# Kernel optimization log

Measured on AMD Instinct MI355X. Metric: run time of the kernel, lower is better.

The kernel has to match this reference:

```python
import jax, jax.numpy as jnp
import numpy as np

B, S, D = 2, 2048, 1024
H = 16
DH = D // H  # 64

def setup_inputs() -> dict:
    key = jax.random.key(0)
    k1, k2, k3, k4 = jax.random.split(key, 4)
    scale = 0.02
    x = jax.random.normal(k1, (B, S, D), dtype=jnp.float32)
    W_query = jax.random.normal(k2, (D, D), dtype=jnp.float32) * scale
    W_key = jax.random.normal(k3, (D, D), dtype=jnp.float32) * scale
    W_value = jax.random.normal(k4, (D, D), dtype=jnp.float32) * scale
    return {"x": x, "W_query": W_query, "W_key": W_key, "W_value": W_value}

def reference(x, W_query, W_key, W_value):
    b, n, d_in = x.shape
    # project and split heads: [b, h, n, dh]
    q = (x @ W_query).reshape(b, n, H, DH).transpose(0, 2, 1, 3)
    k = (x @ W_key).reshape(b, n, H, DH).transpose(0, 2, 1, 3)
    v = (x @ W_value).reshape(b, n, H, DH).transpose(0, 2, 1, 3)
    # raw scores, then causal mask (strict upper triangle -> -inf)
    scores = jnp.einsum('bhqd,bhkd->bhqk', q, k)
    causal = jnp.tril(jnp.ones((n, n), dtype=bool))  # True = keep
    scores = jnp.where(causal, scores, -jnp.inf)
    weights = jax.nn.softmax(scores / jnp.sqrt(jnp.float32(DH)), axis=-1)
    ctx = jnp.einsum('bhqk,bhkd->bhqd', weights, v)
    return ctx.transpose(0, 2, 1, 3).reshape(b, n, H * DH)
```

## Files before the change

kernel.cpp:

```cpp
#include <hip/hip_runtime.h>
#include <hip/hip_bf16.h>

#define S_LEN   2048
#define D_MODEL 1024
#define N_HEADS 16
#define D_HEAD  64
#define HEAD_ELEMS (2048ull * 64ull)
#define MAT_ELEMS  (4096ull * 1024ull)
#define W_ELEMS    (1024ull * 1024ull)

typedef __attribute__((ext_vector_type(8))) short short8_t;
typedef __attribute__((ext_vector_type(4))) short short4_t;
typedef __attribute__((ext_vector_type(4))) float f32x4;

__device__ __forceinline__ short f2bf(float f) {
    __hip_bfloat16 h = __float2bfloat16(f);
    union { __hip_bfloat16 h; short s; } cv;
    cv.h = h;
    return cv.s;
}

#define GLD_LDS16(gptr, lptr) \
    __builtin_amdgcn_global_load_lds( \
        (const __attribute__((address_space(1))) unsigned int*)(gptr), \
        (__attribute__((address_space(3))) unsigned int*)(lptr), 16, 0, 0)

__global__ __launch_bounds__(256) void convert_x_kernel(
    const float* __restrict__ x, short* __restrict__ xb)
{
    const int i = (blockIdx.x * 256 + threadIdx.x) * 8;
    const float4 v0 = *(const float4*)(x + i);
    const float4 v1 = *(const float4*)(x + i + 4);
    short8_t u;
    u[0] = f2bf(v0.x); u[1] = f2bf(v0.y); u[2] = f2bf(v0.z); u[3] = f2bf(v0.w);
    u[4] = f2bf(v1.x); u[5] = f2bf(v1.y); u[6] = f2bf(v1.z); u[7] = f2bf(v1.w);
    *(short8_t*)(xb + i) = u;
}

__global__ __launch_bounds__(256) void transpose_w_kernel(
    const float* __restrict__ Wq, const float* __restrict__ Wk,
    const float* __restrict__ Wv, short* __restrict__ wt)
{
    const int k0 = blockIdx.x * 64;
    const int n0 = blockIdx.y * 64;
    const int which = blockIdx.z;
    const float* W = (which == 0) ? Wq : (which == 1) ? Wk : Wv;
    short* out = wt + (size_t)which * W_ELEMS;

    __shared__ float Ts[64][68];
    const int t = threadIdx.x;
    {
        const int c4 = (t & 15) * 4;
#pragma unroll
        for (int i = 0; i < 4; ++i) {
            const int r = (t >> 4) + i * 16;
            const float4 v = *(const float4*)(W + (size_t)(k0 + r) * D_MODEL + n0 + c4);
            Ts[c4 + 0][r] = v.x; Ts[c4 + 1][r] = v.y;
            Ts[c4 + 2][r] = v.z; Ts[c4 + 3][r] = v.w;
        }
    }
    __syncthreads();
    const int nl = t >> 2;
#pragma unroll
    for (int s = 0; s < 2; ++s) {
        const int koff = (t & 3) * 8 + s * 32;
        short8_t u;
#pragma unroll
        for (int j = 0; j < 8; ++j) u[j] = f2bf(Ts[nl][koff + j]);
        *(short8_t*)(out + (size_t)(n0 + nl) * D_MODEL + k0 + koff) = u;
    }
}

__global__ __launch_bounds__(256, 3) void qkv_mfma_gemm_kernel(
    const short* __restrict__ xb,
    const short* __restrict__ wt,
    short* __restrict__ qkv)
{
    const int mBlock = blockIdx.x * 128;
    const int nBlock = blockIdx.y * 128;
    const int which  = blockIdx.z;
    const short* Bt = wt + (size_t)which * W_ELEMS;
    short* outBase  = qkv + (size_t)which * MAT_ELEMS;

    __shared__ short As[128 * 32];
    __shared__ short Bs[128 * 32];
    __shared__ __align__(16) short Es[4][64 * 72];

    const int t    = threadIdx.x;
    const int w    = t >> 6;
    const int lane = t & 63;
    const int n16  = lane & 15;
    const int quad = lane >> 4;
    const int mq   = (w & 1) * 64;
    const int nq   = (w >> 1) * 64;

    f32x4 acc[4][4];
#pragma unroll
    for (int i = 0; i < 4; ++i)
#pragma unroll
        for (int j = 0; j < 4; ++j) acc[i][j] = (f32x4){0.f, 0.f, 0.f, 0.f};

    const int off0 = w * 2048 + lane * 16;
    const int off1 = off0 + 1024;
    const int r0s = off0 >> 6, k0s = (off0 & 63) >> 1;
    const int r1s = off1 >> 6, k1s = (off1 & 63) >> 1;
    const short* gA0 = xb + (size_t)(mBlock + r0s) * D_MODEL + k0s;
    const short* gA1 = xb + (size_t)(mBlock + r1s) * D_MODEL + k1s;
    const short* gB0 = Bt + (size_t)(nBlock + r0s) * D_MODEL + k0s;
    const short* gB1 = Bt + (size_t)(nBlock + r1s) * D_MODEL + k1s;
    short* lA0 = As + w * 1024;
    short* lA1 = As + w * 1024 + 512;
    short* lB0 = Bs + w * 1024;
    short* lB1 = Bs + w * 1024 + 512;

    for (int k0 = 0; k0 < D_MODEL; k0 += 32) {
        __syncthreads();
        GLD_LDS16(gA0 + k0, lA0);
        GLD_LDS16(gA1 + k0, lA1);
        GLD_LDS16(gB0 + k0, lB0);
        GLD_LDS16(gB1 + k0, lB1);
        __syncthreads();

        short8_t af[4], bf[4];
#pragma unroll
        for (int mt = 0; mt < 4; ++mt)
            af[mt] = *(const short8_t*)&As[(mq + mt * 16 + n16) * 32 + quad * 8];
#pragma unroll
        for (int nt = 0; nt < 4; ++nt)
            bf[nt] = *(const short8_t*)&Bs[(nq + nt * 16 + n16) * 32 + quad * 8];
#pragma unroll
        for (int mt = 0; mt < 4; ++mt)
#pragma unroll
            for (int nt = 0; nt < 4; ++nt)
                acc[mt][nt] = __builtin_amdgcn_mfma_f32_16x16x32_bf16(
                    af[mt], bf[nt], acc[mt][nt], 0, 0, 0);
    }

    const float oscale = (which == 0) ? 0.125f * 1.44269504089f : 1.0f;
    if (which < 2) {
        short* E = &Es[w][0];
#pragma unroll
        for (int mt = 0; mt < 4; ++mt)
#pragma unroll
            for (int nt = 0; nt < 4; ++nt) {
                const int dhl = nt * 16 + n16;
#pragma unroll
                for (int reg = 0; reg < 4; ++reg) {
                    const int ml = mt * 16 + quad * 4 + reg;
                    E[ml * 72 + dhl] = f2bf(acc[mt][nt][reg] * oscale);
                }
            }
        const int h  = (nBlock + nq) >> 6;
        const int m0 = mBlock + mq;
        const int bb = m0 >> 11, ss0 = m0 & 2047;
        const int rsub = lane >> 3;
        const int ch   = lane & 7;
        short* orow = outBase + ((size_t)(bb * N_HEADS + h) * S_LEN + ss0) * D_HEAD
                      + ch * 8;
#pragma unroll
        for (int it = 0; it < 8; ++it) {
            const int row = it * 8 + rsub;
            const short8_t v = *(const short8_t*)&E[row * 72 + ch * 8];
            *(short8_t*)(orow + (size_t)row * D_HEAD) = v;
        }
    } else {
#pragma unroll
        for (int mt = 0; mt < 4; ++mt) {
            const int m0 = mBlock + mq + mt * 16 + quad * 4;
            const int bb = m0 >> 11, ss0 = m0 & 2047;
#pragma unroll
            for (int nt = 0; nt < 4; ++nt) {
                const int n = nBlock + nq + nt * 16 + n16;
                const int h = n >> 6, dh = n & 63;
                short4_t u;
                u[0] = f2bf(acc[mt][nt][0]); u[1] = f2bf(acc[mt][nt][1]);
                u[2] = f2bf(acc[mt][nt][2]); u[3] = f2bf(acc[mt][nt][3]);
                *(short4_t*)(outBase +
                    ((size_t)((bb * N_HEADS + h) * D_HEAD + dh)) * S_LEN + ss0) = u;
            }
        }
    }
}

__global__ __launch_bounds__(256, 4) void attn_mfma_kernel(
    const short* __restrict__ qkv,
    float* __restrict__ out)
{
    const int bh   = blockIdx.x;
    const int qb   = 31 - blockIdx.y;
    const int t    = threadIdx.x;
    const int w    = t >> 6;
    const int lane = t & 63;
    const int n    = lane & 15;
    const int quad = lane >> 4;

    const short* Q  = qkv + (size_t)bh * HEAD_ELEMS;
    const short* K  = qkv + MAT_ELEMS + (size_t)bh * HEAD_ELEMS;
    const short* Vt = qkv + 2 * MAT_ELEMS + (size_t)bh * HEAD_ELEMS;

    __shared__ __align__(16) short Ks[64 * 64];
    __shared__ __align__(16) short Vs[64 * 64];
    __shared__ __align__(16) short Ps[4][16][72];

    const int srow0 = w * 16 + (lane >> 3);
    const int srow1 = srow0 + 8;
    const int sd0 = ((lane & 7) ^ (srow0 & 7)) * 8;
    const int sd1 = ((lane & 7) ^ (srow1 & 7)) * 8;
    const short* gK0 = K + srow0 * 64 + sd0;
    const short* gK1 = K + srow1 * 64 + sd1;
    const short* gV0 = Vt + (size_t)srow0 * S_LEN + sd0;
    const short* gV1 = Vt + (size_t)srow1 * S_LEN + sd1;
    short* lK0 = Ks + (w * 16) * 64;
    short* lK1 = Ks + (w * 16 + 8) * 64;
    short* lV0 = Vs + (w * 16) * 64;
    short* lV1 = Vs + (w * 16 + 8) * 64;

    const int pcK = ((quad ^ (n & 7))) * 8;

    const int bb = bh >> 4;
    const int hh = bh & 15;

    const int r0   = qb * 64 + w * 16;
    const int qrow = r0 + n;

    const short8_t bq0 = *(const short8_t*)(Q + (size_t)qrow * D_HEAD + quad * 8);
    const short8_t bq1 = *(const short8_t*)(Q + (size_t)qrow * D_HEAD + quad * 8 + 32);

    float m = -__builtin_inff();
    float l = 0.f;
    f32x4 o[4];
#pragma unroll
    for (int f = 0; f < 4; ++f) o[f] = (f32x4){0.f, 0.f, 0.f, 0.f};

    for (int tile = 0; tile <= qb; ++tile) {
        const int j0 = tile * 64;
        __syncthreads();
        GLD_LDS16(gK0 + j0 * 64, lK0);
        GLD_LDS16(gK1 + j0 * 64, lK1);
        GLD_LDS16(gV0 + j0, lV0);
        GLD_LDS16(gV1 + j0, lV1);
        __syncthreads();

        f32x4 st[4];
        __builtin_amdgcn_s_setprio(1);
#pragma unroll
        for (int kg = 0; kg < 4; ++kg) {
            const int rbase = (kg * 16 + n) * 64;
            const short8_t a0 = *(const short8_t*)&Ks[rbase + pcK];
            const short8_t a1 = *(const short8_t*)&Ks[rbase + (pcK ^ 32)];
            f32x4 acc = (f32x4){0.f, 0.f, 0.f, 0.f};
            acc = __builtin_amdgcn_mfma_f32_16x16x32_bf16(a0, bq0, acc, 0, 0, 0);
            acc = __builtin_amdgcn_mfma_f32_16x16x32_bf16(a1, bq1, acc, 0, 0, 0);
            st[kg] = acc;
        }
        __builtin_amdgcn_s_setprio(0);

        float p[16];
        float mx = -__builtin_inff();
        if (tile == qb) {
#pragma unroll
            for (int kg = 0; kg < 4; ++kg)
#pragma unroll
                for (int r = 0; r < 4; ++r) {
                    const int key = j0 + kg * 16 + quad * 4 + r;
                    float s = st[kg][r];
                    s = (key <= qrow) ? s : -__builtin_inff();
                    p[kg * 4 + r] = s;
                    mx = fmaxf(mx, s);
                }
        } else {
#pragma unroll
            for (int i = 0; i < 16; ++i) {
                const float s = st[i >> 2][i & 3];
                p[i] = s;
                mx = fmaxf(mx, s);
            }
        }
        mx = fmaxf(mx, __shfl_xor(mx, 16));
        mx = fmaxf(mx, __shfl_xor(mx, 32));

        float ls = 0.f;
        if (__all(mx <= m + 8.0f)) {
#pragma unroll
            for (int i = 0; i < 16; ++i) {
                p[i] = __builtin_amdgcn_exp2f(p[i] - m);
                ls += p[i];
            }
            ls += __shfl_xor(ls, 16);
            ls += __shfl_xor(ls, 32);
            l += ls;
        } else {
            const float mnew  = fmaxf(m, mx);
            const float alpha = __builtin_amdgcn_exp2f(m - mnew);
#pragma unroll
            for (int i = 0; i < 16; ++i) {
                p[i] = __builtin_amdgcn_exp2f(p[i] - mnew);
                ls += p[i];
            }
            ls += __shfl_xor(ls, 16);
            ls += __shfl_xor(ls, 32);
            l = l * alpha + ls;
            m = mnew;
#pragma unroll
            for (int f = 0; f < 4; ++f) {
                o[f][0] *= alpha; o[f][1] *= alpha;
                o[f][2] *= alpha; o[f][3] *= alpha;
            }
        }

#pragma unroll
        for (int kg = 0; kg < 4; ++kg) {
            const unsigned int b0 = __builtin_bit_cast(unsigned int, p[kg * 4 + 0]);
            const unsigned int b1 = __builtin_bit_cast(unsigned int, p[kg * 4 + 1]);
            const unsigned int b2 = __builtin_bit_cast(unsigned int, p[kg * 4 + 2]);
            const unsigned int b3 = __builtin_bit_cast(unsigned int, p[kg * 4 + 3]);
            uint2 pk;
            pk.x = (b0 >> 16) | (b1 & 0xffff0000u);
            pk.y = (b2 >> 16) | (b3 & 0xffff0000u);
            *(uint2*)&Ps[w][n][kg * 16 + quad * 4] = pk;
        }
        const short8_t pb0 = *(const short8_t*)&Ps[w][n][quad * 8];
        const short8_t pb1 = *(const short8_t*)&Ps[w][n][quad * 8 + 32];

        __builtin_amdgcn_s_setprio(1);
#pragma unroll
        for (int f = 0; f < 4; ++f) {
            const int rbase = (f * 16 + n) * 64;
            const short8_t va0 = *(const short8_t*)&Vs[rbase + pcK];
            const short8_t va1 = *(const short8_t*)&Vs[rbase + (pcK ^ 32)];
            o[f] = __builtin_amdgcn_mfma_f32_16x16x32_bf16(va0, pb0, o[f], 0, 0, 0);
            o[f] = __builtin_amdgcn_mfma_f32_16x16x32_bf16(va1, pb1, o[f], 0, 0, 0);
        }
        __builtin_amdgcn_s_setprio(0);
    }

    __syncthreads();
    float* Os = (float*)((w < 2) ? (void*)Ks : (void*)Vs) + (w & 1) * 1024;
    const float inv_l = 1.0f / l;
#pragma unroll
    for (int f = 0; f < 4; ++f) {
        const int c  = f * 4 + quad;
        const int pc = c ^ n;
        f32x4 q4;
        q4[0] = o[f][0] * inv_l; q4[1] = o[f][1] * inv_l;
        q4[2] = o[f][2] * inv_l; q4[3] = o[f][3] * inv_l;
        *(f32x4*)&Os[n * 64 + pc * 4] = q4;
    }
#pragma unroll
    for (int rr = 0; rr < 4; ++rr) {
        const int row = rr * 4 + quad;
        const int pc  = n ^ row;
        const f32x4 val = *(const f32x4*)&Os[row * 64 + pc * 4];
        *(f32x4*)(out + ((size_t)(bb * S_LEN + r0 + row)) * D_MODEL
                      + hh * D_HEAD + n * 4) = val;
    }
}

extern "C" void kernel_launch(void* const* d_in, const int* in_sizes, int n_in,
                              void* d_out, int out_size, void* d_ws, size_t ws_size,
                              hipStream_t stream) {
    const float* x  = (const float*)d_in[0];
    const float* Wq = (const float*)d_in[1];
    const float* Wk = (const float*)d_in[2];
    const float* Wv = (const float*)d_in[3];
    float* out = (float*)d_out;

    short* xb  = (short*)d_ws;
    short* wt  = xb + MAT_ELEMS;
    short* qkv = wt + 3 * W_ELEMS;

    convert_x_kernel<<<dim3(MAT_ELEMS / (256 * 8)), 256, 0, stream>>>(x, xb);
    transpose_w_kernel<<<dim3(16, 16, 3), 256, 0, stream>>>(Wq, Wk, Wv, wt);

    qkv_mfma_gemm_kernel<<<dim3(32, 8, 3), 256, 0, stream>>>(xb, wt, qkv);

    attn_mfma_kernel<<<dim3(32, 32), 256, 0, stream>>>(qkv, out);
}
```

Before: 155.1 us.

## Split KV tiles across two warp groups and pair causal query blocks per CTA

The attention kernel now uses 512 threads split into two 4-wave groups. Each group processes alternating 64-key tiles with its own K/V LDS buffers, and the two partial softmax states are merged through shared memory at the end. Each CTA handles a complementary pair of query blocks (pr and 31-pr), which balances the causal triangle and halves the grid. The goal is better load balance and more in-flight work per CU. The cost is doubled LDS, an extra merge/reduction step, and idle groups in odd rounds.

```diff
diff --git a/kernel.cpp b/kernel.cpp
--- a/kernel.cpp
+++ b/kernel.cpp
@@ -182,14 +182,16 @@
     }
 }
 
-__global__ __launch_bounds__(256, 4) void attn_mfma_kernel(
+__global__ __launch_bounds__(512, 4) void attn_mfma_kernel(
     const short* __restrict__ qkv,
     float* __restrict__ out)
 {
     const int bh   = blockIdx.x;
-    const int qb   = 31 - blockIdx.y;
+    const int pr   = blockIdx.y;
     const int t    = threadIdx.x;
     const int w    = t >> 6;
+    const int g    = w >> 2;
+    const int wl   = w & 3;
     const int lane = t & 63;
     const int n    = lane & 15;
     const int quad = lane >> 4;
@@ -198,11 +200,13 @@
     const short* K  = qkv + MAT_ELEMS + (size_t)bh * HEAD_ELEMS;
     const short* Vt = qkv + 2 * MAT_ELEMS + (size_t)bh * HEAD_ELEMS;
 
-    __shared__ __align__(16) short Ks[64 * 64];
-    __shared__ __align__(16) short Vs[64 * 64];
-    __shared__ __align__(16) short Ps[4][16][72];
-
-    const int srow0 = w * 16 + (lane >> 3);
+    __shared__ __align__(16) short Ks[2][64 * 64];
+    __shared__ __align__(16) short Vs[2][64 * 64];
+    __shared__ __align__(16) short Ps[8][16][72];
+    __shared__ float Ml[2][64];
+    __shared__ float Ll[2][64];
+
+    const int srow0 = wl * 16 + (lane >> 3);
     const int srow1 = srow0 + 8;
     const int sd0 = ((lane & 7) ^ (srow0 & 7)) * 8;
     const int sd1 = ((lane & 7) ^ (srow1 & 7)) * 8;
@@ -210,149 +214,184 @@
     const short* gK1 = K + srow1 * 64 + sd1;
     const short* gV0 = Vt + (size_t)srow0 * S_LEN + sd0;
     const short* gV1 = Vt + (size_t)srow1 * S_LEN + sd1;
-    short* lK0 = Ks + (w * 16) * 64;
-    short* lK1 = Ks + (w * 16 + 8) * 64;
-    short* lV0 = Vs + (w * 16) * 64;
-    short* lV1 = Vs + (w * 16 + 8) * 64;
+    short* lK0 = &Ks[g][(wl * 16) * 64];
+    short* lK1 = &Ks[g][(wl * 16 + 8) * 64];
+    short* lV0 = &Vs[g][(wl * 16) * 64];
+    short* lV1 = &Vs[g][(wl * 16 + 8) * 64];
 
     const int pcK = ((quad ^ (n & 7))) * 8;
 
     const int bb = bh >> 4;
     const int hh = bh & 15;
 
-    const int r0   = qb * 64 + w * 16;
-    const int qrow = r0 + n;
-
-    const short8_t bq0 = *(const short8_t*)(Q + (size_t)qrow * D_HEAD + quad * 8);
-    const short8_t bq1 = *(const short8_t*)(Q + (size_t)qrow * D_HEAD + quad * 8 + 32);
-
-    float m = -__builtin_inff();
-    float l = 0.f;
-    f32x4 o[4];
-#pragma unroll
-    for (int f = 0; f < 4; ++f) o[f] = (f32x4){0.f, 0.f, 0.f, 0.f};
-
-    for (int tile = 0; tile <= qb; ++tile) {
-        const int j0 = tile * 64;
-        __syncthreads();
-        GLD_LDS16(gK0 + j0 * 64, lK0);
-        GLD_LDS16(gK1 + j0 * 64, lK1);
-        GLD_LDS16(gV0 + j0, lV0);
-        GLD_LDS16(gV1 + j0, lV1);
-        __syncthreads();
-
-        f32x4 st[4];
-        __builtin_amdgcn_s_setprio(1);
-#pragma unroll
-        for (int kg = 0; kg < 4; ++kg) {
-            const int rbase = (kg * 16 + n) * 64;
-            const short8_t a0 = *(const short8_t*)&Ks[rbase + pcK];
-            const short8_t a1 = *(const short8_t*)&Ks[rbase + (pcK ^ 32)];
-            f32x4 acc = (f32x4){0.f, 0.f, 0.f, 0.f};
-            acc = __builtin_amdgcn_mfma_f32_16x16x32_bf16(a0, bq0, acc, 0, 0, 0);
-            acc = __builtin_amdgcn_mfma_f32_16x16x32_bf16(a1, bq1, acc, 0, 0, 0);
-            st[kg] = acc;
-        }
-        __builtin_amdgcn_s_setprio(0);
-
-        float p[16];
-        float mx = -__builtin_inff();
-        if (tile == qb) {
-#pragma unroll
-            for (int kg = 0; kg < 4; ++kg)
-#pragma unroll
-                for (int r = 0; r < 4; ++r) {
-                    const int key = j0 + kg * 16 + quad * 4 + r;
-                    float s = st[kg][r];
-                    s = (key <= qrow) ? s : -__builtin_inff();
-                    p[kg * 4 + r] = s;
+    for (int pass = 0; pass < 2; ++pass) {
+        const int qb = pass ? (31 - pr) : pr;
+        const int r0 = qb * 64 + wl * 16;
+        const int qrow = r0 + n;
+
+        const short8_t bq0 = *(const short8_t*)(Q + (size_t)qrow * D_HEAD + quad * 8);
+        const short8_t bq1 = *(const short8_t*)(Q + (size_t)qrow * D_HEAD + quad * 8 + 32);
+
+        float m = -__builtin_inff();
+        float l = 0.f;
+        f32x4 o[4];
+#pragma unroll
+        for (int f = 0; f < 4; ++f) o[f] = (f32x4){0.f, 0.f, 0.f, 0.f};
+
+        const int nrounds = (qb + 2) >> 1;
+        for (int rd = 0; rd < nrounds; ++rd) {
+            const int tg = rd * 2 + g;
+            const bool have = (tg <= qb);
+            const int j0 = tg * 64;
+
+            __syncthreads();
+            if (have) {
+                GLD_LDS16(gK0 + j0 * 64, lK0);
+                GLD_LDS16(gK1 + j0 * 64, lK1);
+                GLD_LDS16(gV0 + j0, lV0);
+                GLD_LDS16(gV1 + j0, lV1);
+            }
+            __syncthreads();
+
+            if (!have) continue;
+
+            f32x4 st[4];
+            __builtin_amdgcn_s_setprio(1);
+#pragma unroll
+            for (int kg = 0; kg < 4; ++kg) {
+                const int rbase = (kg * 16 + n) * 64;
+                const short8_t a0 = *(const short8_t*)&Ks[g][rbase + pcK];
+                const short8_t a1 = *(const short8_t*)&Ks[g][rbase + (pcK ^ 32)];
+                f32x4 acc = (f32x4){0.f, 0.f, 0.f, 0.f};
+                acc = __builtin_amdgcn_mfma_f32_16x16x32_bf16(a0, bq0, acc, 0, 0, 0);
+                acc = __builtin_amdgcn_mfma_f32_16x16x32_bf16(a1, bq1, acc, 0, 0, 0);
+                st[kg] = acc;
+            }
+            __builtin_amdgcn_s_setprio(0);
+
+            float p[16];
+            float mx = -__builtin_inff();
+            if (tg == qb) {
+#pragma unroll
+                for (int kg = 0; kg < 4; ++kg)
+#pragma unroll
+                    for (int r = 0; r < 4; ++r) {
+                        const int key = j0 + kg * 16 + quad * 4 + r;
+                        float s = st[kg][r];
+                        s = (key <= qrow) ? s : -__builtin_inff();
+                        p[kg * 4 + r] = s;
+                        mx = fmaxf(mx, s);
+                    }
+            } else {
+#pragma unroll
+                for (int i = 0; i < 16; ++i) {
+                    const float s = st[i >> 2][i & 3];
+                    p[i] = s;
                     mx = fmaxf(mx, s);
                 }
-        } else {
-#pragma unroll
-            for (int i = 0; i < 16; ++i) {
-                const float s = st[i >> 2][i & 3];
-                p[i] = s;
-                mx = fmaxf(mx, s);
-            }
-        }
-        mx = fmaxf(mx, __shfl_xor(mx, 16));
-        mx = fmaxf(mx, __shfl_xor(mx, 32));
-
-        float ls = 0.f;
-        if (__all(mx <= m + 8.0f)) {
-#pragma unroll
-            for (int i = 0; i < 16; ++i) {
-                p[i] = __builtin_amdgcn_exp2f(p[i] - m);
-                ls += p[i];
-            }
-            ls += __shfl_xor(ls, 16);
-            ls += __shfl_xor(ls, 32);
-            l += ls;
-        } else {
-            const float mnew  = fmaxf(m, mx);
-            const float alpha = __builtin_amdgcn_exp2f(m - mnew);
-#pragma unroll
-            for (int i = 0; i < 16; ++i) {
-                p[i] = __builtin_amdgcn_exp2f(p[i] - mnew);
-                ls += p[i];
-            }
-            ls += __shfl_xor(ls, 16);
-            ls += __shfl_xor(ls, 32);
-            l = l * alpha + ls;
-            m = mnew;
+            }
+            mx = fmaxf(mx, __shfl_xor(mx, 16));
+            mx = fmaxf(mx, __shfl_xor(mx, 32));
+
+            float ls = 0.f;
+            if (__all(mx <= m + 8.0f)) {
+#pragma unroll
+                for (int i = 0; i < 16; ++i) {
+                    p[i] = __builtin_amdgcn_exp2f(p[i] - m);
+                    ls += p[i];
+                }
+                ls += __shfl_xor(ls, 16);
+                ls += __shfl_xor(ls, 32);
+                l += ls;
+            } else {
+                const float mnew  = fmaxf(m, mx);
+                const float alpha = __builtin_amdgcn_exp2f(m - mnew);
+#pragma unroll
+                for (int i = 0; i < 16; ++i) {
+                    p[i] = __builtin_amdgcn_exp2f(p[i] - mnew);
+                    ls += p[i];
+                }
+                ls += __shfl_xor(ls, 16);
+                ls += __shfl_xor(ls, 32);
+                l = l * alpha + ls;
+                m = mnew;
+#pragma unroll
+                for (int f = 0; f < 4; ++f) {
+                    o[f][0] *= alpha; o[f][1] *= alpha;
+                    o[f][2] *= alpha; o[f][3] *= alpha;
+                }
+            }
+
+#pragma unroll
+            for (int kg = 0; kg < 4; ++kg) {
+                const unsigned int b0 = __builtin_bit_cast(unsigned int, p[kg * 4 + 0]);
+                const unsigned int b1 = __builtin_bit_cast(unsigned int, p[kg * 4 + 1]);
+                const unsigned int b2 = __builtin_bit_cast(unsigned int, p[kg * 4 + 2]);
+                const unsigned int b3 = __builtin_bit_cast(unsigned int, p[kg * 4 + 3]);
+                uint2 pk;
+                pk.x = (b0 >> 16) | (b1 & 0xffff0000u);
+                pk.y = (b2 >> 16) | (b3 & 0xffff0000u);
+                *(uint2*)&Ps[w][n][kg * 16 + quad * 4] = pk;
+            }
+            const short8_t pb0 = *(const short8_t*)&Ps[w][n][quad * 8];
+            const short8_t pb1 = *(const short8_t*)&Ps[w][n][quad * 8 + 32];
+
+            __builtin_amdgcn_s_setprio(1);
 #pragma unroll
             for (int f = 0; f < 4; ++f) {
-                o[f][0] *= alpha; o[f][1] *= alpha;
-                o[f][2] *= alpha; o[f][3] *= alpha;
-            }
-        }
-
-#pragma unroll
-        for (int kg = 0; kg < 4; ++kg) {
-            const unsigned int b0 = __builtin_bit_cast(unsigned int, p[kg * 4 + 0]);
-            const unsigned int b1 = __builtin_bit_cast(unsigned int, p[kg * 4 + 1]);
-            const unsigned int b2 = __builtin_bit_cast(unsigned int, p[kg * 4 + 2]);
-            const unsigned int b3 = __builtin_bit_cast(unsigned int, p[kg * 4 + 3]);
-            uint2 pk;
-            pk.x = (b0 >> 16) | (b1 & 0xffff0000u);
-            pk.y = (b2 >> 16) | (b3 & 0xffff0000u);
-            *(uint2*)&Ps[w][n][kg * 16 + quad * 4] = pk;
-        }
-        const short8_t pb0 = *(const short8_t*)&Ps[w][n][quad * 8];
-        const short8_t pb1 = *(const short8_t*)&Ps[w][n][quad * 8 + 32];
-
-        __builtin_amdgcn_s_setprio(1);
-#pragma unroll
-        for (int f = 0; f < 4; ++f) {
-            const int rbase = (f * 16 + n) * 64;
-            const short8_t va0 = *(const short8_t*)&Vs[rbase + pcK];
-            const short8_t va1 = *(const short8_t*)&Vs[rbase + (pcK ^ 32)];
-            o[f] = __builtin_amdgcn_mfma_f32_16x16x32_bf16(va0, pb0, o[f], 0, 0, 0);
-            o[f] = __builtin_amdgcn_mfma_f32_16x16x32_bf16(va1, pb1, o[f], 0, 0, 0);
-        }
-        __builtin_amdgcn_s_setprio(0);
-    }
-
-    __syncthreads();
-    float* Os = (float*)((w < 2) ? (void*)Ks : (void*)Vs) + (w & 1) * 1024;
-    const float inv_l = 1.0f / l;
-#pragma unroll
-    for (int f = 0; f < 4; ++f) {
-        const int c  = f * 4 + quad;
-        const int pc = c ^ n;
-        f32x4 q4;
-        q4[0] = o[f][0] * inv_l; q4[1] = o[f][1] * inv_l;
-        q4[2] = o[f][2] * inv_l; q4[3] = o[f][3] * inv_l;
-        *(f32x4*)&Os[n * 64 + pc * 4] = q4;
-    }
-#pragma unroll
-    for (int rr = 0; rr < 4; ++rr) {
-        const int row = rr * 4 + quad;
-        const int pc  = n ^ row;
-        const f32x4 val = *(const f32x4*)&Os[row * 64 + pc * 4];
-        *(f32x4*)(out + ((size_t)(bb * S_LEN + r0 + row)) * D_MODEL
-                      + hh * D_HEAD + n * 4) = val;
+                const int rbase = (f * 16 + n) * 64;
+                const short8_t va0 = *(const short8_t*)&Vs[g][rbase + pcK];
+                const short8_t va1 = *(const short8_t*)&Vs[g][rbase + (pcK ^ 32)];
+                o[f] = __builtin_amdgcn_mfma_f32_16x16x32_bf16(va0, pb0, o[f], 0, 0, 0);
+                o[f] = __builtin_amdgcn_mfma_f32_16x16x32_bf16(va1, pb1, o[f], 0, 0, 0);
+            }
+            __builtin_amdgcn_s_setprio(0);
+        }
+
+        __syncthreads();
+        {
+            float* Og = (float*)(g == 0 ? (void*)Ks : (void*)Vs) + wl * 1024;
+#pragma unroll
+            for (int f = 0; f < 4; ++f) {
+                const int c  = f * 4 + quad;
+                const int pc = c ^ n;
+                *(f32x4*)&Og[n * 64 + pc * 4] = o[f];
+            }
+            if (quad == 0) {
+                Ml[g][wl * 16 + n] = m;
+                Ll[g][wl * 16 + n] = l;
+            }
+        }
+        __syncthreads();
+        {
+            const int row = t >> 3;
+            const int c8  = t & 7;
+            const int wr  = row >> 4;
+            const int nr_ = row & 15;
+            const float m0 = Ml[0][row], m1 = Ml[1][row];
+            const float l0 = Ll[0][row], l1 = Ll[1][row];
+            const float M  = fmaxf(m0, m1);
+            const float a0 = __builtin_amdgcn_exp2f(m0 - M);
+            const float a1 = __builtin_amdgcn_exp2f(m1 - M);
+            const float inv = 1.0f / (l0 * a0 + l1 * a1);
+            const float* O0 = (const float*)Ks + wr * 1024;
+            const float* O1 = (const float*)Vs + wr * 1024;
+            float* op = out + ((size_t)(bb * S_LEN + qb * 64 + row)) * D_MODEL
+                        + hh * D_HEAD + c8 * 8;
+#pragma unroll
+            for (int cc = 0; cc < 2; ++cc) {
+                const int c  = c8 * 2 + cc;
+                const int pc = c ^ nr_;
+                const f32x4 x0 = *(const f32x4*)&O0[nr_ * 64 + pc * 4];
+                const f32x4 x1 = *(const f32x4*)&O1[nr_ * 64 + pc * 4];
+                f32x4 r;
+                r[0] = (x0[0] * a0 + x1[0] * a1) * inv;
+                r[1] = (x0[1] * a0 + x1[1] * a1) * inv;
+                r[2] = (x0[2] * a0 + x1[2] * a1) * inv;
+                r[3] = (x0[3] * a0 + x1[3] * a1) * inv;
+                *(f32x4*)(op + cc * 4) = r;
+            }
+        }
     }
 }
 
@@ -374,5 +413,5 @@
 
     qkv_mfma_gemm_kernel<<<dim3(32, 8, 3), 256, 0, stream>>>(xb, wt, qkv);
 
-    attn_mfma_kernel<<<dim3(32, 32), 256, 0, stream>>>(qkv, out);
-}
+    attn_mfma_kernel<<<dim3(2 * N_HEADS, 16), 512, 0, stream>>>(qkv, out);
+}
```

New measurement: 149.7 us. -3.5%, faster.

## Process two query blocks per attention workgroup to reuse K/V tiles

Applied to the files above, without the earlier changes.

Each attention workgroup now handles 128 query rows, kept as two 64-row sub-blocks with separate softmax state, instead of 64 rows. Every K/V tile loaded into LDS is therefore used by both sub-blocks, which roughly halves global-to-LDS traffic and barrier count per unit of work. The grid shrinks to half as many workgroups (512), and each thread holds more registers for the second accumulator set. This can lower occupancy and parallelism on a GPU with many compute units.

```diff
diff --git a/kernel.cpp b/kernel.cpp
--- a/kernel.cpp
+++ b/kernel.cpp
@@ -187,7 +187,7 @@
     float* __restrict__ out)
 {
     const int bh   = blockIdx.x;
-    const int qb   = 31 - blockIdx.y;
+    const int qb   = 15 - blockIdx.y;
     const int t    = threadIdx.x;
     const int w    = t >> 6;
     const int lane = t & 63;
@@ -220,20 +220,26 @@
     const int bb = bh >> 4;
     const int hh = bh & 15;
 
-    const int r0   = qb * 64 + w * 16;
-    const int qrow = r0 + n;
-
-    const short8_t bq0 = *(const short8_t*)(Q + (size_t)qrow * D_HEAD + quad * 8);
-    const short8_t bq1 = *(const short8_t*)(Q + (size_t)qrow * D_HEAD + quad * 8 + 32);
-
-    float m = -__builtin_inff();
-    float l = 0.f;
-    f32x4 o[4];
-#pragma unroll
-    for (int f = 0; f < 4; ++f) o[f] = (f32x4){0.f, 0.f, 0.f, 0.f};
-
-    for (int tile = 0; tile <= qb; ++tile) {
-        const int j0 = tile * 64;
+    const int r0a   = qb * 128 + w * 16;
+    const int qrow0 = r0a + n;
+    const int qrow1 = qrow0 + 64;
+
+    const short8_t bq00 = *(const short8_t*)(Q + (size_t)qrow0 * D_HEAD + quad * 8);
+    const short8_t bq01 = *(const short8_t*)(Q + (size_t)qrow0 * D_HEAD + quad * 8 + 32);
+    const short8_t bq10 = *(const short8_t*)(Q + (size_t)qrow1 * D_HEAD + quad * 8);
+    const short8_t bq11 = *(const short8_t*)(Q + (size_t)qrow1 * D_HEAD + quad * 8 + 32);
+
+    float mm[2] = {-__builtin_inff(), -__builtin_inff()};
+    float ll[2] = {0.f, 0.f};
+    f32x4 oo[2][4];
+#pragma unroll
+    for (int s = 0; s < 2; ++s)
+#pragma unroll
+        for (int f = 0; f < 4; ++f) oo[s][f] = (f32x4){0.f, 0.f, 0.f, 0.f};
+
+    const int ntiles = 2 * qb + 2;
+    for (int tg = 0; tg < ntiles; ++tg) {
+        const int j0 = tg * 64;
         __syncthreads();
         GLD_LDS16(gK0 + j0 * 64, lK0);
         GLD_LDS16(gK1 + j0 * 64, lK1);
@@ -241,118 +247,129 @@
         GLD_LDS16(gV1 + j0, lV1);
         __syncthreads();
 
-        f32x4 st[4];
-        __builtin_amdgcn_s_setprio(1);
-#pragma unroll
-        for (int kg = 0; kg < 4; ++kg) {
-            const int rbase = (kg * 16 + n) * 64;
-            const short8_t a0 = *(const short8_t*)&Ks[rbase + pcK];
-            const short8_t a1 = *(const short8_t*)&Ks[rbase + (pcK ^ 32)];
-            f32x4 acc = (f32x4){0.f, 0.f, 0.f, 0.f};
-            acc = __builtin_amdgcn_mfma_f32_16x16x32_bf16(a0, bq0, acc, 0, 0, 0);
-            acc = __builtin_amdgcn_mfma_f32_16x16x32_bf16(a1, bq1, acc, 0, 0, 0);
-            st[kg] = acc;
-        }
-        __builtin_amdgcn_s_setprio(0);
-
-        float p[16];
-        float mx = -__builtin_inff();
-        if (tile == qb) {
-#pragma unroll
-            for (int kg = 0; kg < 4; ++kg)
-#pragma unroll
-                for (int r = 0; r < 4; ++r) {
-                    const int key = j0 + kg * 16 + quad * 4 + r;
-                    float s = st[kg][r];
-                    s = (key <= qrow) ? s : -__builtin_inff();
-                    p[kg * 4 + r] = s;
+#pragma unroll
+        for (int sub = 0; sub < 2; ++sub) {
+            if (sub == 0 && tg == ntiles - 1) continue;
+            const int qrow = sub ? qrow1 : qrow0;
+            const short8_t bqa = sub ? bq10 : bq00;
+            const short8_t bqb = sub ? bq11 : bq01;
+
+            f32x4 st[4];
+            __builtin_amdgcn_s_setprio(1);
+#pragma unroll
+            for (int kg = 0; kg < 4; ++kg) {
+                const int rbase = (kg * 16 + n) * 64;
+                const short8_t a0 = *(const short8_t*)&Ks[rbase + pcK];
+                const short8_t a1 = *(const short8_t*)&Ks[rbase + (pcK ^ 32)];
+                f32x4 acc = (f32x4){0.f, 0.f, 0.f, 0.f};
+                acc = __builtin_amdgcn_mfma_f32_16x16x32_bf16(a0, bqa, acc, 0, 0, 0);
+                acc = __builtin_amdgcn_mfma_f32_16x16x32_bf16(a1, bqb, acc, 0, 0, 0);
+                st[kg] = acc;
+            }
+            __builtin_amdgcn_s_setprio(0);
+
+            float p[16];
+            float mx = -__builtin_inff();
+            if (tg == 2 * qb + sub) {
+#pragma unroll
+                for (int kg = 0; kg < 4; ++kg)
+#pragma unroll
+                    for (int r = 0; r < 4; ++r) {
+                        const int key = j0 + kg * 16 + quad * 4 + r;
+                        float s = st[kg][r];
+                        s = (key <= qrow) ? s : -__builtin_inff();
+                        p[kg * 4 + r] = s;
+                        mx = fmaxf(mx, s);
+                    }
+            } else {
+#pragma unroll
+                for (int i = 0; i < 16; ++i) {
+                    const float s = st[i >> 2][i & 3];
+                    p[i] = s;
                     mx = fmaxf(mx, s);
                 }
-        } else {
-#pragma unroll
-            for (int i = 0; i < 16; ++i) {
-                const float s = st[i >> 2][i & 3];
-                p[i] = s;
-                mx = fmaxf(mx, s);
-            }
-        }
-        mx = fmaxf(mx, __shfl_xor(mx, 16));
-        mx = fmaxf(mx, __shfl_xor(mx, 32));
-
-        float ls = 0.f;
-        if (__all(mx <= m + 8.0f)) {
-#pragma unroll
-            for (int i = 0; i < 16; ++i) {
-                p[i] = __builtin_amdgcn_exp2f(p[i] - m);
-                ls += p[i];
-            }
-            ls += __shfl_xor(ls, 16);
-            ls += __shfl_xor(ls, 32);
-            l += ls;
-        } else {
-            const float mnew  = fmaxf(m, mx);
-            const float alpha = __builtin_amdgcn_exp2f(m - mnew);
-#pragma unroll
-            for (int i = 0; i < 16; ++i) {
-                p[i] = __builtin_amdgcn_exp2f(p[i] - mnew);
-                ls += p[i];
-            }
-            ls += __shfl_xor(ls, 16);
-            ls += __shfl_xor(ls, 32);
-            l = l * alpha + ls;
-            m = mnew;
+            }
+            mx = fmaxf(mx, __shfl_xor(mx, 16));
+            mx = fmaxf(mx, __shfl_xor(mx, 32));
+
+            float ls = 0.f;
+            if (__all(mx <= mm[sub] + 8.0f)) {
+#pragma unroll
+                for (int i = 0; i < 16; ++i) {
+                    p[i] = __builtin_amdgcn_exp2f(p[i] - mm[sub]);
+                    ls += p[i];
+                }
+                ls += __shfl_xor(ls, 16);
+                ls += __shfl_xor(ls, 32);
+                ll[sub] += ls;
+            } else {
+                const float mnew  = fmaxf(mm[sub], mx);
+                const float alpha = __builtin_amdgcn_exp2f(mm[sub] - mnew);
+#pragma unroll
+                for (int i = 0; i < 16; ++i) {
+                    p[i] = __builtin_amdgcn_exp2f(p[i] - mnew);
+                    ls += p[i];
+                }
+                ls += __shfl_xor(ls, 16);
+                ls += __shfl_xor(ls, 32);
+                ll[sub] = ll[sub] * alpha + ls;
+                mm[sub] = mnew;
+#pragma unroll
+                for (int f = 0; f < 4; ++f) {
+                    oo[sub][f][0] *= alpha; oo[sub][f][1] *= alpha;
+                    oo[sub][f][2] *= alpha; oo[sub][f][3] *= alpha;
+                }
+            }
+
+#pragma unroll
+            for (int kg = 0; kg < 4; ++kg) {
+                const unsigned int b0 = __builtin_bit_cast(unsigned int, p[kg * 4 + 0]);
+                const unsigned int b1 = __builtin_bit_cast(unsigned int, p[kg * 4 + 1]);
+                const unsigned int b2 = __builtin_bit_cast(unsigned int, p[kg * 4 + 2]);
+                const unsigned int b3 = __builtin_bit_cast(unsigned int, p[kg * 4 + 3]);
+                uint2 pk;
+                pk.x = (b0 >> 16) | (b1 & 0xffff0000u);
+                pk.y = (b2 >> 16) | (b3 & 0xffff0000u);
+                *(uint2*)&Ps[w][n][kg * 16 + quad * 4] = pk;
+            }
+            const short8_t pb0 = *(const short8_t*)&Ps[w][n][quad * 8];
+            const short8_t pb1 = *(const short8_t*)&Ps[w][n][quad * 8 + 32];
+
+            __builtin_amdgcn_s_setprio(1);
 #pragma unroll
             for (int f = 0; f < 4; ++f) {
-                o[f][0] *= alpha; o[f][1] *= alpha;
-                o[f][2] *= alpha; o[f][3] *= alpha;
-            }
-        }
-
-#pragma unroll
-        for (int kg = 0; kg < 4; ++kg) {
-            const unsigned int b0 = __builtin_bit_cast(unsigned int, p[kg * 4 + 0]);
-            const unsigned int b1 = __builtin_bit_cast(unsigned int, p[kg * 4 + 1]);
-            const unsigned int b2 = __builtin_bit_cast(unsigned int, p[kg * 4 + 2]);
-            const unsigned int b3 = __builtin_bit_cast(unsigned int, p[kg * 4 + 3]);
-            uint2 pk;
-            pk.x = (b0 >> 16) | (b1 & 0xffff0000u);
-            pk.y = (b2 >> 16) | (b3 & 0xffff0000u);
-            *(uint2*)&Ps[w][n][kg * 16 + quad * 4] = pk;
-        }
-        const short8_t pb0 = *(const short8_t*)&Ps[w][n][quad * 8];
-        const short8_t pb1 = *(const short8_t*)&Ps[w][n][quad * 8 + 32];
-
-        __builtin_amdgcn_s_setprio(1);
-#pragma unroll
-        for (int f = 0; f < 4; ++f) {
-            const int rbase = (f * 16 + n) * 64;
-            const short8_t va0 = *(const short8_t*)&Vs[rbase + pcK];
-            const short8_t va1 = *(const short8_t*)&Vs[rbase + (pcK ^ 32)];
-            o[f] = __builtin_amdgcn_mfma_f32_16x16x32_bf16(va0, pb0, o[f], 0, 0, 0);
-            o[f] = __builtin_amdgcn_mfma_f32_16x16x32_bf16(va1, pb1, o[f], 0, 0, 0);
-        }
-        __builtin_amdgcn_s_setprio(0);
+                const int rbase = (f * 16 + n) * 64;
+                const short8_t va0 = *(const short8_t*)&Vs[rbase + pcK];
+                const short8_t va1 = *(const short8_t*)&Vs[rbase + (pcK ^ 32)];
+                oo[sub][f] = __builtin_amdgcn_mfma_f32_16x16x32_bf16(va0, pb0, oo[sub][f], 0, 0, 0);
+                oo[sub][f] = __builtin_amdgcn_mfma_f32_16x16x32_bf16(va1, pb1, oo[sub][f], 0, 0, 0);
+            }
+            __builtin_amdgcn_s_setprio(0);
+        }
     }
 
     __syncthreads();
     float* Os = (float*)((w < 2) ? (void*)Ks : (void*)Vs) + (w & 1) * 1024;
-    const float inv_l = 1.0f / l;
-#pragma unroll
-    for (int f = 0; f < 4; ++f) {
-        const int c  = f * 4 + quad;
-        const int pc = c ^ n;
-        f32x4 q4;
-        q4[0] = o[f][0] * inv_l; q4[1] = o[f][1] * inv_l;
-        q4[2] = o[f][2] * inv_l; q4[3] = o[f][3] * inv_l;
-        *(f32x4*)&Os[n * 64 + pc * 4] = q4;
-    }
-#pragma unroll
-    for (int rr = 0; rr < 4; ++rr) {
-        const int row = rr * 4 + quad;
-        const int pc  = n ^ row;
-        const f32x4 val = *(const f32x4*)&Os[row * 64 + pc * 4];
-        *(f32x4*)(out + ((size_t)(bb * S_LEN + r0 + row)) * D_MODEL
-                      + hh * D_HEAD + n * 4) = val;
+#pragma unroll
+    for (int sub = 0; sub < 2; ++sub) {
+        const float inv_l = 1.0f / ll[sub];
+#pragma unroll
+        for (int f = 0; f < 4; ++f) {
+            const int c  = f * 4 + quad;
+            const int pc = c ^ n;
+            f32x4 q4;
+            q4[0] = oo[sub][f][0] * inv_l; q4[1] = oo[sub][f][1] * inv_l;
+            q4[2] = oo[sub][f][2] * inv_l; q4[3] = oo[sub][f][3] * inv_l;
+            *(f32x4*)&Os[n * 64 + pc * 4] = q4;
+        }
+#pragma unroll
+        for (int rr = 0; rr < 4; ++rr) {
+            const int row = rr * 4 + quad;
+            const int pc  = n ^ row;
+            const f32x4 val = *(const f32x4*)&Os[row * 64 + pc * 4];
+            *(f32x4*)(out + ((size_t)(bb * S_LEN + r0a + sub * 64 + row)) * D_MODEL
+                          + hh * D_HEAD + n * 4) = val;
+        }
     }
 }
 
@@ -374,5 +391,5 @@
 
     qkv_mfma_gemm_kernel<<<dim3(32, 8, 3), 256, 0, stream>>>(xb, wt, qkv);
 
-    attn_mfma_kernel<<<dim3(32, 32), 256, 0, stream>>>(qkv, out);
-}
+    attn_mfma_kernel<<<dim3(32, 16), 256, 0, stream>>>(qkv, out);
+}
```

After: 171.9 us. 10.9% more time.

## Split attention keys across waves, pair causal query blocks, stage V transpose store

Applied to the files above, without the earlier changes.

The attention kernel now assigns each wave a 16-key slice of every K/V tile rather than 16 query rows. Each wave computes scores for all 64 queries with register-held P fed to 16x16x16 MFMAs, and the per-wave partial softmax state is merged through shared memory at the end. Each block processes a light and a heavy causal query block (pr and 31-pr) for load balance, and the grid halves. The V-transposed GEMM epilogue now stages through LDS to make coalesced 16-byte stores. This adds a cross-wave reduction with several barriers, higher register pressure (occupancy bound lowered to 2), and inline asm MFMA.

```diff
diff --git a/kernel.cpp b/kernel.cpp
--- a/kernel.cpp
+++ b/kernel.cpp
@@ -18,6 +18,13 @@
     union { __hip_bfloat16 h; short s; } cv;
     cv.h = h;
     return cv.s;
+}
+
+__device__ __forceinline__ f32x4 mfma16_bf16(short4_t a, short4_t b, f32x4 c) {
+    f32x4 d;
+    asm("v_mfma_f32_16x16x16_bf16 %0, %1, %2, %3"
+        : "=v"(d) : "v"(a), "v"(b), "0"(c));
+    return d;
 }
 
 #define GLD_LDS16(gptr, lptr) \
@@ -137,8 +144,14 @@
     }
 
     const float oscale = (which == 0) ? 0.125f * 1.44269504089f : 1.0f;
+    short* E = &Es[w][0];
+    const int h  = (nBlock + nq) >> 6;
+    const int m0 = mBlock + mq;
+    const int bb = m0 >> 11, ss0 = m0 & 2047;
+    const int rsub = lane >> 3;
+    const int ch   = lane & 7;
+
     if (which < 2) {
-        short* E = &Es[w][0];
 #pragma unroll
         for (int mt = 0; mt < 4; ++mt)
 #pragma unroll
@@ -150,11 +163,6 @@
                     E[ml * 72 + dhl] = f2bf(acc[mt][nt][reg] * oscale);
                 }
             }
-        const int h  = (nBlock + nq) >> 6;
-        const int m0 = mBlock + mq;
-        const int bb = m0 >> 11, ss0 = m0 & 2047;
-        const int rsub = lane >> 3;
-        const int ch   = lane & 7;
         short* orow = outBase + ((size_t)(bb * N_HEADS + h) * S_LEN + ss0) * D_HEAD
                       + ch * 8;
 #pragma unroll
@@ -165,29 +173,33 @@
         }
     } else {
 #pragma unroll
-        for (int mt = 0; mt < 4; ++mt) {
-            const int m0 = mBlock + mq + mt * 16 + quad * 4;
-            const int bb = m0 >> 11, ss0 = m0 & 2047;
+        for (int mt = 0; mt < 4; ++mt)
 #pragma unroll
             for (int nt = 0; nt < 4; ++nt) {
-                const int n = nBlock + nq + nt * 16 + n16;
-                const int h = n >> 6, dh = n & 63;
+                const int dhl = nt * 16 + n16;
+                const int sl0 = mt * 16 + quad * 4;
                 short4_t u;
                 u[0] = f2bf(acc[mt][nt][0]); u[1] = f2bf(acc[mt][nt][1]);
                 u[2] = f2bf(acc[mt][nt][2]); u[3] = f2bf(acc[mt][nt][3]);
-                *(short4_t*)(outBase +
-                    ((size_t)((bb * N_HEADS + h) * D_HEAD + dh)) * S_LEN + ss0) = u;
-            }
+                *(short4_t*)&E[dhl * 72 + sl0] = u;
+            }
+        short* orow = outBase + ((size_t)(bb * N_HEADS + h) * D_HEAD) * S_LEN
+                      + ss0 + ch * 8;
+#pragma unroll
+        for (int it = 0; it < 8; ++it) {
+            const int dhl = it * 8 + rsub;
+            const short8_t v = *(const short8_t*)&E[dhl * 72 + ch * 8];
+            *(short8_t*)(orow + (size_t)dhl * S_LEN) = v;
         }
     }
 }
 
-__global__ __launch_bounds__(256, 4) void attn_mfma_kernel(
+__global__ __launch_bounds__(256, 2) void attn_mfma_kernel(
     const short* __restrict__ qkv,
     float* __restrict__ out)
 {
     const int bh   = blockIdx.x;
-    const int qb   = 31 - blockIdx.y;
+    const int pr   = blockIdx.y;
     const int t    = threadIdx.x;
     const int w    = t >> 6;
     const int lane = t & 63;
@@ -200,7 +212,9 @@
 
     __shared__ __align__(16) short Ks[64 * 64];
     __shared__ __align__(16) short Vs[64 * 64];
-    __shared__ __align__(16) short Ps[4][16][72];
+    __shared__ __align__(16) float Ob[64 * 68];
+    __shared__ float Mw[4][64];
+    __shared__ float Lw[4][64];
 
     const int srow0 = w * 16 + (lane >> 3);
     const int srow1 = srow0 + 8;
@@ -216,143 +230,198 @@
     short* lV1 = Vs + (w * 16 + 8) * 64;
 
     const int pcK = ((quad ^ (n & 7))) * 8;
+    const int vphys = ((2 * w + (quad >> 1)) ^ (n & 7)) * 8 + (quad & 1) * 4;
 
     const int bb = bh >> 4;
     const int hh = bh & 15;
-
-    const int r0   = qb * 64 + w * 16;
-    const int qrow = r0 + n;
-
-    const short8_t bq0 = *(const short8_t*)(Q + (size_t)qrow * D_HEAD + quad * 8);
-    const short8_t bq1 = *(const short8_t*)(Q + (size_t)qrow * D_HEAD + quad * 8 + 32);
-
-    float m = -__builtin_inff();
-    float l = 0.f;
-    f32x4 o[4];
-#pragma unroll
-    for (int f = 0; f < 4; ++f) o[f] = (f32x4){0.f, 0.f, 0.f, 0.f};
-
-    for (int tile = 0; tile <= qb; ++tile) {
-        const int j0 = tile * 64;
+    const int kw = 16 * w + quad * 4;
+
+    for (int pass = 0; pass < 2; ++pass) {
+        const int qb = pass ? (31 - pr) : pr;
+
+        short8_t bq[4][2];
+#pragma unroll
+        for (int qg = 0; qg < 4; ++qg) {
+            const short* qp = Q + (size_t)(qb * 64 + qg * 16 + n) * D_HEAD + quad * 8;
+            bq[qg][0] = *(const short8_t*)(qp);
+            bq[qg][1] = *(const short8_t*)(qp + 32);
+        }
+
+        float m[4], l[4];
+        f32x4 o[4][4];
+#pragma unroll
+        for (int qg = 0; qg < 4; ++qg) { m[qg] = -1e30f; l[qg] = 0.f; }
+#pragma unroll
+        for (int f = 0; f < 4; ++f)
+#pragma unroll
+            for (int qg = 0; qg < 4; ++qg) o[f][qg] = (f32x4){0.f, 0.f, 0.f, 0.f};
+
+        for (int tile = 0; tile <= qb; ++tile) {
+            const int j0 = tile * 64;
+            __syncthreads();
+            GLD_LDS16(gK0 + j0 * 64, lK0);
+            GLD_LDS16(gK1 + j0 * 64, lK1);
+            GLD_LDS16(gV0 + j0, lV0);
+            GLD_LDS16(gV1 + j0, lV1);
+            __syncthreads();
+
+            const int krow = (16 * w + n) * 64;
+            const short8_t a0 = *(const short8_t*)&Ks[krow + pcK];
+            const short8_t a1 = *(const short8_t*)&Ks[krow + (pcK ^ 32)];
+            f32x4 st[4];
+            __builtin_amdgcn_s_setprio(1);
+#pragma unroll
+            for (int qg = 0; qg < 4; ++qg) {
+                f32x4 acc = (f32x4){0.f, 0.f, 0.f, 0.f};
+                acc = __builtin_amdgcn_mfma_f32_16x16x32_bf16(a0, bq[qg][0], acc, 0, 0, 0);
+                acc = __builtin_amdgcn_mfma_f32_16x16x32_bf16(a1, bq[qg][1], acc, 0, 0, 0);
+                st[qg] = acc;
+            }
+            __builtin_amdgcn_s_setprio(0);
+
+            float mx[4];
+            const bool diag = (tile == qb);
+#pragma unroll
+            for (int qg = 0; qg < 4; ++qg) {
+                if (diag) {
+#pragma unroll
+                    for (int r = 0; r < 4; ++r)
+                        st[qg][r] = (kw + r <= qg * 16 + n) ? st[qg][r]
+                                                            : -__builtin_inff();
+                }
+                float mxq = fmaxf(fmaxf(st[qg][0], st[qg][1]),
+                                  fmaxf(st[qg][2], st[qg][3]));
+                mxq = fmaxf(mxq, __shfl_xor(mxq, 16));
+                mxq = fmaxf(mxq, __shfl_xor(mxq, 32));
+                mx[qg] = fmaxf(mxq, -1e30f);
+            }
+
+            const bool ok = (mx[0] <= m[0] + 8.0f) && (mx[1] <= m[1] + 8.0f) &&
+                            (mx[2] <= m[2] + 8.0f) && (mx[3] <= m[3] + 8.0f);
+            float pv[4][4];
+            if (__all(ok)) {
+#pragma unroll
+                for (int qg = 0; qg < 4; ++qg) {
+                    float ls = 0.f;
+#pragma unroll
+                    for (int r = 0; r < 4; ++r) {
+                        pv[qg][r] = __builtin_amdgcn_exp2f(st[qg][r] - m[qg]);
+                        ls += pv[qg][r];
+                    }
+                    ls += __shfl_xor(ls, 16);
+                    ls += __shfl_xor(ls, 32);
+                    l[qg] += ls;
+                }
+            } else {
+#pragma unroll
+                for (int qg = 0; qg < 4; ++qg) {
+                    const float mnew  = fmaxf(m[qg], mx[qg]);
+                    const float alpha = __builtin_amdgcn_exp2f(m[qg] - mnew);
+                    float ls = 0.f;
+#pragma unroll
+                    for (int r = 0; r < 4; ++r) {
+                        pv[qg][r] = __builtin_amdgcn_exp2f(st[qg][r] - mnew);
+                        ls += pv[qg][r];
+                    }
+                    ls += __shfl_xor(ls, 16);
+                    ls += __shfl_xor(ls, 32);
+                    l[qg] = l[qg] * alpha + ls;
+                    m[qg] = mnew;
+#pragma unroll
+                    for (int f = 0; f < 4; ++f) {
+                        o[f][qg][0] *= alpha; o[f][qg][1] *= alpha;
+                        o[f][qg][2] *= alpha; o[f][qg][3] *= alpha;
+                    }
+                }
+            }
+
+            short4_t pf[4];
+#pragma unroll
+            for (int qg = 0; qg < 4; ++qg) {
+                const unsigned int b0 = __builtin_bit_cast(unsigned int, pv[qg][0]);
+                const unsigned int b1 = __builtin_bit_cast(unsigned int, pv[qg][1]);
+                const unsigned int b2 = __builtin_bit_cast(unsigned int, pv[qg][2]);
+                const unsigned int b3 = __builtin_bit_cast(unsigned int, pv[qg][3]);
+                uint2 pk;
+                pk.x = (b0 >> 16) | (b1 & 0xffff0000u);
+                pk.y = (b2 >> 16) | (b3 & 0xffff0000u);
+                pf[qg] = __builtin_bit_cast(short4_t, pk);
+            }
+
+            __builtin_amdgcn_s_setprio(1);
+#pragma unroll
+            for (int f = 0; f < 4; ++f) {
+                const short4_t va = *(const short4_t*)&Vs[(f * 16 + n) * 64 + vphys];
+#pragma unroll
+                for (int qg = 0; qg < 4; ++qg)
+                    o[f][qg] = mfma16_bf16(va, pf[qg], o[f][qg]);
+            }
+            __builtin_amdgcn_s_setprio(0);
+        }
+
         __syncthreads();
-        GLD_LDS16(gK0 + j0 * 64, lK0);
-        GLD_LDS16(gK1 + j0 * 64, lK1);
-        GLD_LDS16(gV0 + j0, lV0);
-        GLD_LDS16(gV1 + j0, lV1);
+        if (quad == 0) {
+#pragma unroll
+            for (int qg = 0; qg < 4; ++qg) {
+                Mw[w][qg * 16 + n] = m[qg];
+                Lw[w][qg * 16 + n] = l[qg];
+            }
+        }
         __syncthreads();
-
-        f32x4 st[4];
-        __builtin_amdgcn_s_setprio(1);
-#pragma unroll
-        for (int kg = 0; kg < 4; ++kg) {
-            const int rbase = (kg * 16 + n) * 64;
-            const short8_t a0 = *(const short8_t*)&Ks[rbase + pcK];
-            const short8_t a1 = *(const short8_t*)&Ks[rbase + (pcK ^ 32)];
-            f32x4 acc = (f32x4){0.f, 0.f, 0.f, 0.f};
-            acc = __builtin_amdgcn_mfma_f32_16x16x32_bf16(a0, bq0, acc, 0, 0, 0);
-            acc = __builtin_amdgcn_mfma_f32_16x16x32_bf16(a1, bq1, acc, 0, 0, 0);
-            st[kg] = acc;
-        }
-        __builtin_amdgcn_s_setprio(0);
-
-        float p[16];
-        float mx = -__builtin_inff();
-        if (tile == qb) {
-#pragma unroll
-            for (int kg = 0; kg < 4; ++kg)
-#pragma unroll
-                for (int r = 0; r < 4; ++r) {
-                    const int key = j0 + kg * 16 + quad * 4 + r;
-                    float s = st[kg][r];
-                    s = (key <= qrow) ? s : -__builtin_inff();
-                    p[kg * 4 + r] = s;
-                    mx = fmaxf(mx, s);
+        float aw[4];
+#pragma unroll
+        for (int qg = 0; qg < 4; ++qg) {
+            const int q = qg * 16 + n;
+            const float M = fmaxf(fmaxf(Mw[0][q], Mw[1][q]),
+                                  fmaxf(Mw[2][q], Mw[3][q]));
+            aw[qg] = __builtin_amdgcn_exp2f(m[qg] - M);
+        }
+#pragma unroll
+        for (int f = 0; f < 4; ++f)
+#pragma unroll
+            for (int qg = 0; qg < 4; ++qg) {
+                o[f][qg][0] *= aw[qg]; o[f][qg][1] *= aw[qg];
+                o[f][qg][2] *= aw[qg]; o[f][qg][3] *= aw[qg];
+            }
+#pragma unroll
+        for (int rr = 0; rr < 4; ++rr) {
+            const int qg = w ^ rr;
+            if (rr == 0) {
+#pragma unroll
+                for (int f = 0; f < 4; ++f)
+                    *(f32x4*)&Ob[(qg * 16 + n) * 68 + f * 16 + quad * 4] = o[f][qg];
+            } else {
+#pragma unroll
+                for (int f = 0; f < 4; ++f) {
+                    float* pOb = &Ob[(qg * 16 + n) * 68 + f * 16 + quad * 4];
+                    f32x4 x = *(f32x4*)pOb;
+                    x[0] += o[f][qg][0]; x[1] += o[f][qg][1];
+                    x[2] += o[f][qg][2]; x[3] += o[f][qg][3];
+                    *(f32x4*)pOb = x;
                 }
-        } else {
-#pragma unroll
-            for (int i = 0; i < 16; ++i) {
-                const float s = st[i >> 2][i & 3];
-                p[i] = s;
-                mx = fmaxf(mx, s);
-            }
-        }
-        mx = fmaxf(mx, __shfl_xor(mx, 16));
-        mx = fmaxf(mx, __shfl_xor(mx, 32));
-
-        float ls = 0.f;
-        if (__all(mx <= m + 8.0f)) {
-#pragma unroll
-            for (int i = 0; i < 16; ++i) {
-                p[i] = __builtin_amdgcn_exp2f(p[i] - m);
-                ls += p[i];
-            }
-            ls += __shfl_xor(ls, 16);
-            ls += __shfl_xor(ls, 32);
-            l += ls;
-        } else {
-            const float mnew  = fmaxf(m, mx);
-            const float alpha = __builtin_amdgcn_exp2f(m - mnew);
-#pragma unroll
-            for (int i = 0; i < 16; ++i) {
-                p[i] = __builtin_amdgcn_exp2f(p[i] - mnew);
-                ls += p[i];
-            }
-            ls += __shfl_xor(ls, 16);
-            ls += __shfl_xor(ls, 32);
-            l = l * alpha + ls;
-            m = mnew;
-#pragma unroll
-            for (int f = 0; f < 4; ++f) {
-                o[f][0] *= alpha; o[f][1] *= alpha;
-                o[f][2] *= alpha; o[f][3] *= alpha;
-            }
-        }
-
-#pragma unroll
-        for (int kg = 0; kg < 4; ++kg) {
-            const unsigned int b0 = __builtin_bit_cast(unsigned int, p[kg * 4 + 0]);
-            const unsigned int b1 = __builtin_bit_cast(unsigned int, p[kg * 4 + 1]);
-            const unsigned int b2 = __builtin_bit_cast(unsigned int, p[kg * 4 + 2]);
-            const unsigned int b3 = __builtin_bit_cast(unsigned int, p[kg * 4 + 3]);
-            uint2 pk;
-            pk.x = (b0 >> 16) | (b1 & 0xffff0000u);
-            pk.y = (b2 >> 16) | (b3 & 0xffff0000u);
-            *(uint2*)&Ps[w][n][kg * 16 + quad * 4] = pk;
-        }
-        const short8_t pb0 = *(const short8_t*)&Ps[w][n][quad * 8];
-        const short8_t pb1 = *(const short8_t*)&Ps[w][n][quad * 8 + 32];
-
-        __builtin_amdgcn_s_setprio(1);
-#pragma unroll
-        for (int f = 0; f < 4; ++f) {
-            const int rbase = (f * 16 + n) * 64;
-            const short8_t va0 = *(const short8_t*)&Vs[rbase + pcK];
-            const short8_t va1 = *(const short8_t*)&Vs[rbase + (pcK ^ 32)];
-            o[f] = __builtin_amdgcn_mfma_f32_16x16x32_bf16(va0, pb0, o[f], 0, 0, 0);
-            o[f] = __builtin_amdgcn_mfma_f32_16x16x32_bf16(va1, pb1, o[f], 0, 0, 0);
-        }
-        __builtin_amdgcn_s_setprio(0);
-    }
-
-    __syncthreads();
-    float* Os = (float*)((w < 2) ? (void*)Ks : (void*)Vs) + (w & 1) * 1024;
-    const float inv_l = 1.0f / l;
-#pragma unroll
-    for (int f = 0; f < 4; ++f) {
-        const int c  = f * 4 + quad;
-        const int pc = c ^ n;
-        f32x4 q4;
-        q4[0] = o[f][0] * inv_l; q4[1] = o[f][1] * inv_l;
-        q4[2] = o[f][2] * inv_l; q4[3] = o[f][3] * inv_l;
-        *(f32x4*)&Os[n * 64 + pc * 4] = q4;
-    }
-#pragma unroll
-    for (int rr = 0; rr < 4; ++rr) {
-        const int row = rr * 4 + quad;
-        const int pc  = n ^ row;
-        const f32x4 val = *(const f32x4*)&Os[row * 64 + pc * 4];
-        *(f32x4*)(out + ((size_t)(bb * S_LEN + r0 + row)) * D_MODEL
-                      + hh * D_HEAD + n * 4) = val;
+            }
+            __syncthreads();
+        }
+
+        {
+            const int row = t >> 2;
+            const int c   = t & 3;
+            const float M = fmaxf(fmaxf(Mw[0][row], Mw[1][row]),
+                                  fmaxf(Mw[2][row], Mw[3][row]));
+            float lt = 0.f;
+#pragma unroll
+            for (int wv = 0; wv < 4; ++wv)
+                lt += __builtin_amdgcn_exp2f(Mw[wv][row] - M) * Lw[wv][row];
+            const float inv = 1.0f / lt;
+            float* op = out + ((size_t)(bb * S_LEN + qb * 64 + row)) * D_MODEL
+                        + hh * D_HEAD + c * 16;
+#pragma unroll
+            for (int j = 0; j < 4; ++j) {
+                f32x4 x = *(f32x4*)&Ob[row * 68 + c * 16 + j * 4];
+                x[0] *= inv; x[1] *= inv; x[2] *= inv; x[3] *= inv;
+                *(f32x4*)(op + j * 4) = x;
+            }
+        }
     }
 }
 
@@ -374,5 +443,5 @@
 
     qkv_mfma_gemm_kernel<<<dim3(32, 8, 3), 256, 0, stream>>>(xb, wt, qkv);
 
-    attn_mfma_kernel<<<dim3(32, 32), 256, 0, stream>>>(qkv, out);
-}
+    attn_mfma_kernel<<<dim3(2 * N_HEADS, 16), 256, 0, stream>>>(qkv, out);
+}
```

New measurement: 311.2 us. +100.7%, slower.
